# Optimization experiments

Hardware: AMD Instinct MI355X
Metric: run time of the kernel (lower is better)

The kernel has to match this reference:

```python
import jax, jax.numpy as jnp
import numpy as np

D = 128      # d_model
ED = 256     # d_inner = 2*d_model
N = 16       # d_state
DT = 8       # dt_rank = ceil(d_model/16)
K = 4        # d_conv
NL = 2       # n_layers
NC = 2       # n_classes
EPS = 1e-5


def setup_inputs() -> dict:
    key = jax.random.key(0)
    ks = jax.random.split(key, 16)
    L, IN = 12000, 1024
    s = 0.02
    inp = {}
    inp['x'] = jax.random.normal(ks[0], (1, L, IN), jnp.float32)
    inp['coords'] = jax.random.uniform(ks[1], (L, 2), jnp.float32)
    inp['fc1_w'] = jax.random.normal(ks[2], (IN, D), jnp.float32) * s
    inp['fc1_b'] = jnp.zeros((D,), jnp.float32)
    inp['rms_w'] = jnp.ones((NL, D), jnp.float32)
    inp['inproj_w'] = jax.random.normal(ks[3], (NL, D, 2 * ED), jnp.float32) * s
    inp['conv_w'] = jax.random.normal(ks[4], (NL, ED, K), jnp.float32) * s
    inp['conv_b'] = jnp.zeros((NL, ED), jnp.float32)
    inp['xproj_w'] = jax.random.normal(ks[5], (NL, ED, DT + 2 * N), jnp.float32) * s
    inp['dt_w'] = jax.random.normal(ks[6], (NL, DT, ED), jnp.float32) * s
    inp['dt_b'] = jax.random.normal(ks[7], (NL, ED), jnp.float32) * 0.1
    inp['A_log'] = jnp.log(jnp.broadcast_to(jnp.arange(1, N + 1, dtype=jnp.float32), (NL, ED, N)))
    inp['D_p'] = jnp.ones((NL, ED), jnp.float32)
    inp['outproj_w'] = jax.random.normal(ks[8], (NL, ED, D), jnp.float32) * s
    inp['ln_w'] = jnp.ones((D,), jnp.float32)
    inp['ln_b'] = jnp.zeros((D,), jnp.float32)
    inp['att_w1'] = jax.random.normal(ks[9], (D, 128), jnp.float32) * s
    inp['att_b1'] = jnp.zeros((128,), jnp.float32)
    inp['att_w2'] = jax.random.normal(ks[10], (128, 1), jnp.float32) * s
    inp['att_b2'] = jnp.zeros((1,), jnp.float32)
    inp['cls_w'] = jax.random.normal(ks[11], (D, NC), jnp.float32) * s
    inp['cls_b'] = jnp.zeros((NC,), jnp.float32)
    return inp


def _rmsnorm(x, w):
    return x * jax.lax.rsqrt(jnp.mean(x * x, axis=-1, keepdims=True) + EPS) * w


def _layernorm(x, w, b):
    m = jnp.mean(x, axis=-1, keepdims=True)
    v = jnp.mean((x - m) ** 2, axis=-1, keepdims=True)
    return (x - m) * jax.lax.rsqrt(v + EPS) * w + b


def _causal_conv(xb, w, b):
    # xb: [B,L,ED], w: [ED,K] depthwise causal conv
    xpad = jnp.pad(xb, ((0, 0), (K - 1, 0), (0, 0)))
    kern = w.T[:, None, :]  # [K,1,ED]
    out = jax.lax.conv_general_dilated(
        xpad, kern, window_strides=(1,), padding='VALID',
        feature_group_count=ED, dimension_numbers=('NWC', 'WIO', 'NWC'))
    return out + b


def _mamba_block(h, ipw, cw, cb, xpw, dtw, dtb, alog, dp, opw):
    # h: [B,L,D]
    xz = h @ ipw                                  # [B,L,2*ED]
    xb, z = xz[..., :ED], xz[..., ED:]
    xc = jax.nn.silu(_causal_conv(xb, cw, cb))    # [B,L,ED]
    dbl = xc @ xpw                                # [B,L,DT+2N]
    dlt, Bm, Cm = dbl[..., :DT], dbl[..., DT:DT + N], dbl[..., DT + N:]
    delta = jax.nn.softplus(dlt @ dtw + dtb)      # [B,L,ED]
    A = -jnp.exp(alog)                            # [ED,N]
    dA = jnp.exp(delta[..., None] * A)            # [B,L,ED,N]
    dBx = (delta * xc)[..., None] * Bm[:, :, None, :]

    def step(hs, inp):
        da, dbx, c = inp
        hs = da * hs + dbx                        # [B,ED,N]
        y = jnp.einsum('ben,bn->be', hs, c)
        return hs, y

    h0 = jnp.zeros((dA.shape[0], ED, N), dA.dtype)
    xs = (dA.transpose(1, 0, 2, 3), dBx.transpose(1, 0, 2, 3), Cm.transpose(1, 0, 2))
    _, ys = jax.lax.scan(step, h0, xs)            # [L,B,ED]
    y = ys.transpose(1, 0, 2) + dp * xc
    y = y * jax.nn.silu(z)
    return y @ opw                                # [B,L,D]


def reference(x, coords, fc1_w, fc1_b, rms_w, inproj_w, conv_w, conv_b, xproj_w,
              dt_w, dt_b, A_log, D_p, outproj_w, ln_w, ln_b,
              att_w1, att_b1, att_w2, att_b2, cls_w, cls_b):
    h = jax.nn.gelu(x @ fc1_w + fc1_b, approximate=False)
    for i in range(NL):
        h = h + _mamba_block(_rmsnorm(h, rms_w[i]), inproj_w[i], conv_w[i], conv_b[i],
                             xproj_w[i], dt_w[i], dt_b[i], A_log[i], D_p[i], outproj_w[i])
    h = _layernorm(h, ln_w, ln_b)
    A = jnp.tanh(h @ att_w1 + att_b1) @ att_w2 + att_b2   # [1,L,1]
    A = jax.nn.softmax(A.transpose(0, 2, 1), axis=-1)     # [1,1,L]
    pooled = jnp.einsum('bol,bld->bod', A, h)[0]          # [1,D]
    logits = pooled @ cls_w + cls_b                       # [1,NC]
    Y_prob = jax.nn.softmax(logits, axis=1)
    Y_hat = jnp.argmax(logits, axis=1)
    return (logits, Y_prob, Y_hat)
```

## Files before the change

kernel.cpp:

```cpp
#include <hip/hip_runtime.h>

#define LQ 12000
#define IN_D 1024
#define DM 128
#define EDM 256
#define NS 16
#define CCH 480
#define SCH 25
#define GN 32
#define GSZ 15

typedef __bf16 v8bf __attribute__((ext_vector_type(8)));
typedef float v4f __attribute__((ext_vector_type(4)));

__device__ __forceinline__ float wave_sum64(float v) {
#pragma unroll
  for (int o = 32; o > 0; o >>= 1) v += __shfl_xor(v, o);
  return v;
}
__device__ __forceinline__ float wave_max64(float v) {
#pragma unroll
  for (int o = 32; o > 0; o >>= 1) v = fmaxf(v, __shfl_xor(v, o));
  return v;
}

template <bool AF32, int KT, int NT, int EPI>
__global__ __launch_bounds__(256) void bgemm_k(
    const void* __restrict__ Av, const __bf16* __restrict__ Bt,
    const float* __restrict__ bias, const float* __restrict__ nw,
    const float* __restrict__ nb, const float* __restrict__ hin,
    float* __restrict__ o0, __bf16* __restrict__ o1) {
  constexpr int KCH = KT / 4;
  constexpr int COLS = NT * 32;
  constexpr int RS = COLS + 4;
  constexpr int PL = 32 * RS;
  constexpr int CPT = COLS / 8;
  __shared__ __align__(16) float lds[4 * PL];
  const int tid = threadIdx.x, lane = tid & 63, wid = tid >> 6;
  const int frow = lane & 15, g = lane >> 4, fseg = g * 8;
  const int r0 = blockIdx.x * 32;
  const int k0 = wid * KCH + fseg;

  const float* pa32_0 = nullptr;
  const float* pa32_1 = nullptr;
  const __bf16* pab_0 = nullptr;
  const __bf16* pab_1 = nullptr;
  if constexpr (AF32) {
    pa32_0 = (const float*)Av + (size_t)(r0 + frow) * KT + k0;
    pa32_1 = pa32_0 + (size_t)16 * KT;
  } else {
    pab_0 = (const __bf16*)Av + (size_t)(r0 + frow) * KT + k0;
    pab_1 = pab_0 + (size_t)16 * KT;
  }
  const __bf16* pb[NT][2];
#pragma unroll
  for (int nt = 0; nt < NT; ++nt) {
    pb[nt][0] = Bt + (size_t)(nt * 32 + frow) * KT + k0;
    pb[nt][1] = pb[nt][0] + (size_t)16 * KT;
  }

  v4f acc[NT][2][2] = {};
#pragma unroll
  for (int kt = 0; kt < KCH; kt += 32) {
    v8bf a0, a1;
    if constexpr (AF32) {
      float4 u0 = *(const float4*)(pa32_0 + kt);
      float4 u1 = *(const float4*)(pa32_0 + kt + 4);
      float4 u2 = *(const float4*)(pa32_1 + kt);
      float4 u3 = *(const float4*)(pa32_1 + kt + 4);
      a0 = v8bf{(__bf16)u0.x, (__bf16)u0.y, (__bf16)u0.z, (__bf16)u0.w,
                (__bf16)u1.x, (__bf16)u1.y, (__bf16)u1.z, (__bf16)u1.w};
      a1 = v8bf{(__bf16)u2.x, (__bf16)u2.y, (__bf16)u2.z, (__bf16)u2.w,
                (__bf16)u3.x, (__bf16)u3.y, (__bf16)u3.z, (__bf16)u3.w};
    } else {
      a0 = *(const v8bf*)(pab_0 + kt);
      a1 = *(const v8bf*)(pab_1 + kt);
    }
#pragma unroll
    for (int nt = 0; nt < NT; ++nt) {
      v8bf b0 = *(const v8bf*)(pb[nt][0] + kt);
      v8bf b1 = *(const v8bf*)(pb[nt][1] + kt);
      acc[nt][0][0] =
          __builtin_amdgcn_mfma_f32_16x16x32_bf16(a0, b0, acc[nt][0][0], 0, 0, 0);
      acc[nt][0][1] =
          __builtin_amdgcn_mfma_f32_16x16x32_bf16(a0, b1, acc[nt][0][1], 0, 0, 0);
      acc[nt][1][0] =
          __builtin_amdgcn_mfma_f32_16x16x32_bf16(a1, b0, acc[nt][1][0], 0, 0, 0);
      acc[nt][1][1] =
          __builtin_amdgcn_mfma_f32_16x16x32_bf16(a1, b1, acc[nt][1][1], 0, 0, 0);
    }
  }

  float* pl = lds + wid * PL;
#pragma unroll
  for (int nt = 0; nt < NT; ++nt)
#pragma unroll
    for (int i = 0; i < 2; ++i)
#pragma unroll
      for (int j = 0; j < 2; ++j) {
        int cc = nt * 32 + j * 16 + frow;
#pragma unroll
        for (int r = 0; r < 4; ++r)
          pl[(i * 16 + g * 4 + r) * RS + cc] = acc[nt][i][j][r];
      }
  __syncthreads();

  const int row = tid >> 3, c0 = (tid & 7) * CPT;
  const int rr = r0 + row;
  float v[CPT];
#pragma unroll
  for (int k4 = 0; k4 < CPT / 4; ++k4) {
    v4f s = {0.f, 0.f, 0.f, 0.f};
#pragma unroll
    for (int p = 0; p < 4; ++p)
      s = s + *(const v4f*)&lds[p * PL + row * RS + c0 + k4 * 4];
    v[k4 * 4 + 0] = s[0];
    v[k4 * 4 + 1] = s[1];
    v[k4 * 4 + 2] = s[2];
    v[k4 * 4 + 3] = s[3];
  }

  if constexpr (EPI == 0) {
#pragma unroll
    for (int k = 0; k < CPT; ++k) {
      int c = c0 + k;
      if (c < 40) o0[(size_t)rr * 40 + c] = v[k];
    }
  } else if constexpr (EPI == 1 || EPI == 2) {
    float ss = 0.f;
#pragma unroll
    for (int k = 0; k < CPT; ++k) {
      int c = c0 + k;
      float a;
      if constexpr (EPI == 1) {
        a = v[k] + bias[c];
        a = 0.5f * a * (1.f + erff(a * 0.70710678118654752f));
      } else {
        a = v[k] + hin[(size_t)rr * DM + c];
      }
      v[k] = a;
      o0[(size_t)rr * DM + c] = a;
      ss = fmaf(a, a, ss);
    }
#pragma unroll
    for (int o = 1; o < 8; o <<= 1) ss += __shfl_xor(ss, o);
    float r = 1.f / sqrtf(ss * (1.f / DM) + 1e-5f);
#pragma unroll
    for (int k = 0; k < CPT; ++k) {
      int c = c0 + k;
      o1[(size_t)rr * DM + c] = (__bf16)(v[k] * r * nw[c]);
    }
  } else if constexpr (EPI == 3) {
    float s1 = 0.f, s2 = 0.f;
#pragma unroll
    for (int k = 0; k < CPT; ++k) {
      float a = v[k] + hin[(size_t)rr * DM + c0 + k];
      v[k] = a;
      s1 += a;
      s2 = fmaf(a, a, s2);
    }
#pragma unroll
    for (int o = 1; o < 8; o <<= 1) {
      s1 += __shfl_xor(s1, o);
      s2 += __shfl_xor(s2, o);
    }
    float m = s1 * (1.f / DM);
    float var = s2 * (1.f / DM) - m * m;
    float r = 1.f / sqrtf(var + 1e-5f);
#pragma unroll
    for (int k = 0; k < CPT; ++k) {
      int c = c0 + k;
      float y = (v[k] - m) * r * nw[c] + nb[c];
      o0[(size_t)rr * DM + c] = y;
      o1[(size_t)rr * DM + c] = (__bf16)y;
    }
  } else if constexpr (EPI == 4) {
    float dot = 0.f;
#pragma unroll
    for (int k = 0; k < CPT; ++k) {
      int c = c0 + k;
      float a = tanhf(v[k] + bias[c]);
      dot = fmaf(a, nw[c], dot);
    }
#pragma unroll
    for (int o = 1; o < 8; o <<= 1) dot += __shfl_xor(dot, o);
    if ((tid & 7) == 0) o0[rr] = dot + nb[0];
  }
}

template <int KT>
__global__ __launch_bounds__(256) void wgemm_k(const __bf16* __restrict__ Av,
                                               const __bf16* __restrict__ Bt,
                                               __bf16* __restrict__ Cv, int Mt,
                                               int Nt, int Cs) {
  const int tid = threadIdx.x;
  const int lane = tid & 63;
  const int w = blockIdx.x * 4 + (tid >> 6);
  const int nt = w % Nt;
  const int mt = w / Nt;
  const int frow = lane & 15, fseg = (lane >> 4) * 8;
  const int r0 = mt * 32, c0 = nt * 32;

  const __bf16* pb0 = Bt + (size_t)(c0 + frow) * KT + fseg;
  const __bf16* pb1 = pb0 + (size_t)16 * KT;
  const __bf16* pa0 = Av + (size_t)(r0 + frow) * KT + fseg;
  const __bf16* pa1 = pa0 + (size_t)16 * KT;

  v4f acc[2][2] = {};
#pragma unroll
  for (int kt = 0; kt < KT; kt += 32) {
    v8bf a0 = *(const v8bf*)(pa0 + kt);
    v8bf a1 = *(const v8bf*)(pa1 + kt);
    v8bf b0 = *(const v8bf*)(pb0 + kt);
    v8bf b1 = *(const v8bf*)(pb1 + kt);
    acc[0][0] = __builtin_amdgcn_mfma_f32_16x16x32_bf16(a0, b0, acc[0][0], 0, 0, 0);
    acc[0][1] = __builtin_amdgcn_mfma_f32_16x16x32_bf16(a0, b1, acc[0][1], 0, 0, 0);
    acc[1][0] = __builtin_amdgcn_mfma_f32_16x16x32_bf16(a1, b0, acc[1][0], 0, 0, 0);
    acc[1][1] = __builtin_amdgcn_mfma_f32_16x16x32_bf16(a1, b1, acc[1][1], 0, 0, 0);
  }
#pragma unroll
  for (int i = 0; i < 2; ++i)
#pragma unroll
    for (int j = 0; j < 2; ++j) {
      int cc = c0 + j * 16 + (lane & 15);
#pragma unroll
      for (int r = 0; r < 4; ++r) {
        int rr = r0 + i * 16 + (lane >> 4) * 4 + r;
        Cv[(size_t)rr * Cs + cc] = (__bf16)acc[i][j][r];
      }
    }
}

__global__ __launch_bounds__(256) void castw_k(const float* __restrict__ fc1w,
                                               const float* __restrict__ ipw,
                                               const float* __restrict__ xpw,
                                               const float* __restrict__ opw,
                                               const float* __restrict__ a1w,
                                               __bf16* __restrict__ wp) {
  int idx = blockIdx.x * 256 + threadIdx.x;
  const float* src;
  int K, N, o, base;
  if (idx < 131072) {
    base = 0; o = idx; src = fc1w; K = 1024; N = 128;
  } else if (idx < 262144) {
    int t = idx - 131072; int s = t >> 16; o = t & 65535;
    src = ipw + (size_t)s * 65536; K = 128; N = 512; base = 131072 + (s << 16);
  } else if (idx < 327680) {
    int t = idx - 262144; int s = t >> 15; o = t & 32767;
    src = xpw + (size_t)s * 10240; K = 256; N = 40; base = 262144 + (s << 15);
  } else if (idx < 393216) {
    int t = idx - 327680; int s = t >> 15; o = t & 32767;
    src = opw + (size_t)s * 32768; K = 256; N = 128; base = 327680 + (s << 15);
  } else {
    base = 393216; o = idx - 393216; src = a1w; K = 128; N = 128;
  }
  int n = o / K, k = o - n * K;
  float v = (n < N) ? src[(size_t)k * N + n] : 0.f;
  wp[base + o] = (__bf16)v;
}

__global__ __launch_bounds__(256) void conv_silu_k(const __bf16* __restrict__ xzb,
                                                   const float* __restrict__ cw,
                                                   const float* __restrict__ cb,
                                                   float* __restrict__ xc,
                                                   __bf16* __restrict__ xcb) {
  int idx = blockIdx.x * 256 + threadIdx.x;
  int e = idx & (EDM - 1);
  int t = idx >> 8;
  float acc = cb[e];
  const float* wp = cw + e * 4;
#pragma unroll
  for (int j = 0; j < 4; ++j) {
    int ts = t - 3 + j;
    if (ts >= 0) acc = fmaf((float)xzb[(size_t)ts * 512 + e], wp[j], acc);
  }
  float v = __fdividef(acc, 1.f + __expf(-acc));
  xc[idx] = v;
  xcb[idx] = (__bf16)v;
}


__global__ __launch_bounds__(256) void scan1_k(const float* __restrict__ xc,
                                               const float* __restrict__ dbl,
                                               const float* __restrict__ dtw,
                                               const float* __restrict__ dtb,
                                               float* __restrict__ Dsum,
                                               float* __restrict__ Bacc) {
  int e = threadIdx.x;
  int c = blockIdx.x;
  int t0 = c * SCH;
  float wdt[8];
#pragma unroll
  for (int k = 0; k < 8; ++k) wdt[k] = dtw[k * 256 + e];
  float bdt = dtb[e];
  float h[NS];
#pragma unroll
  for (int n = 0; n < NS; ++n) h[n] = 0.f;
  float ds = 0.f;
  const float* xp = xc + (size_t)t0 * EDM + e;
  const float* rp = dbl + (size_t)t0 * 40;
  for (int s = 0; s < SCH; ++s) {
    const float* R = rp + s * 40;
    float acc = bdt;
#pragma unroll
    for (int k = 0; k < 8; ++k) acc = fmaf(R[k], wdt[k], acc);
    float d = fmaxf(acc, 0.f) + log1pf(expf(-fabsf(acc)));
    float xcv = xp[s * EDM];
    float q = __expf(-d);
    float dx = d * xcv;
    ds += d;
    const float* B = R + 8;
    float p1 = q, p2 = q * q;
    float p3 = p1 * p2, p4 = p2 * p2;
    float p5 = p1 * p4, p6 = p2 * p4, p7 = p3 * p4, p8 = p4 * p4;
    float pw[16] = {p1,      p2,      p3,      p4,      p5,      p6,
                    p7,      p8,      p1 * p8, p2 * p8, p3 * p8, p4 * p8,
                    p5 * p8, p6 * p8, p7 * p8, p8 * p8};
#pragma unroll
    for (int n = 0; n < NS; ++n) h[n] = fmaf(pw[n], h[n], dx * B[n]);
  }
  Dsum[c * EDM + e] = ds;
  float4* bq = (float4*)(Bacc + (size_t)c * 4096 + e * NS);
  bq[0] = make_float4(h[0], h[1], h[2], h[3]);
  bq[1] = make_float4(h[4], h[5], h[6], h[7]);
  bq[2] = make_float4(h[8], h[9], h[10], h[11]);
  bq[3] = make_float4(h[12], h[13], h[14], h[15]);
}

__global__ __launch_bounds__(256) void scan2a_k(const float* __restrict__ alog,
                                                const float* __restrict__ Dsum,
                                                const float* __restrict__ Bacc,
                                                float* __restrict__ Gs,
                                                float* __restrict__ Gb) {
  int b = blockIdx.x;
  int g = b >> 4;
  int ch = ((b & 15) << 8) + threadIdx.x;
  int e = ch >> 4;
  float Aen = -expf(alog[ch]);
  float hh = 0.f, ds = 0.f;
#pragma unroll
  for (int j = 0; j < GSZ; ++j) {
    int c = g * GSZ + j;
    float dsv = Dsum[c * EDM + e];
    ds += dsv;
    hh = fmaf(__expf(Aen * dsv), hh, Bacc[(size_t)c * 4096 + ch]);
  }
  Gs[g * 4096 + ch] = ds;
  Gb[g * 4096 + ch] = hh;
}

__global__ __launch_bounds__(256) void scan2b_k(const float* __restrict__ alog,
                                                const float* __restrict__ Gs,
                                                const float* __restrict__ Gb,
                                                float* __restrict__ Gc) {
  int ch = blockIdx.x * 256 + threadIdx.x;
  float Aen = -expf(alog[ch]);
  float gs[GN], gb[GN];
#pragma unroll
  for (int g = 0; g < GN; ++g) {
    gs[g] = Gs[g * 4096 + ch];
    gb[g] = Gb[g * 4096 + ch];
  }
  float carry = 0.f;
#pragma unroll
  for (int g = 0; g < GN; ++g) {
    Gc[g * 4096 + ch] = carry;
    carry = fmaf(__expf(Aen * gs[g]), carry, gb[g]);
  }
}

__global__ __launch_bounds__(256) void scan2c_k(const float* __restrict__ alog,
                                                const float* __restrict__ Dsum,
                                                float* __restrict__ Bacc,
                                                const float* __restrict__ Gc) {
  int b = blockIdx.x;
  int g = b >> 4;
  int ch = ((b & 15) << 8) + threadIdx.x;
  int e = ch >> 4;
  float Aen = -expf(alog[ch]);
  float carry = Gc[g * 4096 + ch];
#pragma unroll
  for (int j = 0; j < GSZ; ++j) {
    int c = g * GSZ + j;
    float a = __expf(Aen * Dsum[c * EDM + e]);
    float old = Bacc[(size_t)c * 4096 + ch];
    Bacc[(size_t)c * 4096 + ch] = carry;
    carry = fmaf(a, carry, old);
  }
}

__global__ __launch_bounds__(256) void scan3_k(const float* __restrict__ xc,
                                               const float* __restrict__ dbl,
                                               const __bf16* __restrict__ xzb,
                                               const float* __restrict__ Bacc,
                                               const float* __restrict__ dtw,
                                               const float* __restrict__ dtb,
                                               const float* __restrict__ dpw,
                                               __bf16* __restrict__ yb) {
  int e = threadIdx.x;
  int c = blockIdx.x;
  int t0 = c * SCH;
  float wdt[8];
#pragma unroll
  for (int k = 0; k < 8; ++k) wdt[k] = dtw[k * 256 + e];
  float bdt = dtb[e];
  float h[NS];
  const float4* hq = (const float4*)(Bacc + (size_t)c * 4096 + e * NS);
  float4 h0 = hq[0], h1 = hq[1], h2 = hq[2], h3 = hq[3];
  h[0] = h0.x; h[1] = h0.y; h[2] = h0.z; h[3] = h0.w;
  h[4] = h1.x; h[5] = h1.y; h[6] = h1.z; h[7] = h1.w;
  h[8] = h2.x; h[9] = h2.y; h[10] = h2.z; h[11] = h2.w;
  h[12] = h3.x; h[13] = h3.y; h[14] = h3.z; h[15] = h3.w;
  float dpe = dpw[e];
  const float* xp = xc + (size_t)t0 * EDM + e;
  const float* rp = dbl + (size_t)t0 * 40;
  const __bf16* zp = xzb + (size_t)t0 * 512 + 256 + e;
  for (int s = 0; s < SCH; ++s) {
    const float* R = rp + s * 40;
    float acc = bdt;
#pragma unroll
    for (int k = 0; k < 8; ++k) acc = fmaf(R[k], wdt[k], acc);
    float d = fmaxf(acc, 0.f) + log1pf(expf(-fabsf(acc)));
    float xcv = xp[s * EDM];
    float q = __expf(-d);
    float dx = d * xcv;
    const float* B = R + 8;
    const float* Cc = R + 24;
    float p1 = q, p2 = q * q;
    float p3 = p1 * p2, p4 = p2 * p2;
    float p5 = p1 * p4, p6 = p2 * p4, p7 = p3 * p4, p8 = p4 * p4;
    float pw[16] = {p1,      p2,      p3,      p4,      p5,      p6,
                    p7,      p8,      p1 * p8, p2 * p8, p3 * p8, p4 * p8,
                    p5 * p8, p6 * p8, p7 * p8, p8 * p8};
    float v0 = 0.f, v1 = 0.f, v2 = 0.f, v3 = 0.f;
#pragma unroll
    for (int n = 0; n < NS; n += 4) {
      h[n] = fmaf(pw[n], h[n], dx * B[n]);
      v0 = fmaf(h[n], Cc[n], v0);
      h[n + 1] = fmaf(pw[n + 1], h[n + 1], dx * B[n + 1]);
      v1 = fmaf(h[n + 1], Cc[n + 1], v1);
      h[n + 2] = fmaf(pw[n + 2], h[n + 2], dx * B[n + 2]);
      v2 = fmaf(h[n + 2], Cc[n + 2], v2);
      h[n + 3] = fmaf(pw[n + 3], h[n + 3], dx * B[n + 3]);
      v3 = fmaf(h[n + 3], Cc[n + 3], v3);
    }
    float v = (v0 + v1) + (v2 + v3);
    float y = v + dpe * xcv;
    float z = (float)zp[s * 512];
    y *= __fdividef(z, 1.f + __expf(-z));
    yb[(size_t)(t0 + s) * EDM + e] = (__bf16)y;
  }
}

__global__ __launch_bounds__(1024) void att_stats_k(const float* __restrict__ s,
                                                    float* __restrict__ stats) {
  __shared__ float red[16];
  int lane = threadIdx.x & 63, wid = threadIdx.x >> 6;
  float m = -1e30f;
  for (int i = threadIdx.x; i < LQ; i += 1024) m = fmaxf(m, s[i]);
  m = wave_max64(m);
  if (lane == 0) red[wid] = m;
  __syncthreads();
  if (threadIdx.x < 16) {
    float mm = red[threadIdx.x];
#pragma unroll
    for (int o = 8; o > 0; o >>= 1) mm = fmaxf(mm, __shfl_xor(mm, o));
    if (threadIdx.x == 0) red[0] = mm;
  }
  __syncthreads();
  float smax = red[0];
  __syncthreads();
  float sum = 0.f;
  for (int i = threadIdx.x; i < LQ; i += 1024) sum += expf(s[i] - smax);
  sum = wave_sum64(sum);
  if (lane == 0) red[wid] = sum;
  __syncthreads();
  if (threadIdx.x == 0) {
    float tot = 0.f;
    for (int i = 0; i < 16; ++i) tot += red[i];
    stats[0] = smax;
    stats[1] = tot;
  }
}

__global__ __launch_bounds__(128) void pooled_k(const float* __restrict__ s,
                                                const float* __restrict__ stats,
                                                const float* __restrict__ hn,
                                                float* __restrict__ pooled) {
  __shared__ float w[64];
  int t0 = blockIdx.x * 64;
  float smax = stats[0];
  if (threadIdx.x < 64) {
    int t = t0 + threadIdx.x;
    w[threadIdx.x] = (t < LQ) ? expf(s[t] - smax) : 0.f;
  }
  __syncthreads();
  int d = threadIdx.x;
  float acc = 0.f;
  int nmax = min(64, LQ - t0);
  for (int i = 0; i < nmax; ++i)
    acc = fmaf(w[i], hn[(size_t)(t0 + i) * DM + d], acc);
  atomicAdd(&pooled[d], acc);
}

__global__ __launch_bounds__(128) void final_k(const float* __restrict__ pooled,
                                               const float* __restrict__ stats,
                                               const float* __restrict__ cls_w,
                                               const float* __restrict__ cls_b,
                                               float* __restrict__ out) {
  __shared__ float r0[2], r1[2];
  int lane = threadIdx.x & 63, wid = threadIdx.x >> 6;
  float p = pooled[threadIdx.x] / stats[1];
  float v0 = p * cls_w[threadIdx.x * 2 + 0];
  float v1 = p * cls_w[threadIdx.x * 2 + 1];
  v0 = wave_sum64(v0);
  v1 = wave_sum64(v1);
  if (lane == 0) {
    r0[wid] = v0;
    r1[wid] = v1;
  }
  __syncthreads();
  if (threadIdx.x == 0) {
    float L0 = r0[0] + r0[1] + cls_b[0];
    float L1 = r1[0] + r1[1] + cls_b[1];
    float mx = fmaxf(L0, L1);
    float e0 = expf(L0 - mx), e1 = expf(L1 - mx);
    float inv = 1.f / (e0 + e1);
    out[0] = L0;
    out[1] = L1;
    out[2] = e0 * inv;
    out[3] = e1 * inv;
    out[4] = (L1 > L0) ? 1.f : 0.f;
  }
}

extern "C" void kernel_launch(void* const* d_in, const int* in_sizes, int n_in,
                              void* d_out, int out_size, void* d_ws,
                              size_t ws_size, hipStream_t stream) {
  const float* x = (const float*)d_in[0];
  const float* fc1_w = (const float*)d_in[2];
  const float* fc1_b = (const float*)d_in[3];
  const float* rms_w = (const float*)d_in[4];
  const float* inproj_w = (const float*)d_in[5];
  const float* conv_w = (const float*)d_in[6];
  const float* conv_b = (const float*)d_in[7];
  const float* xproj_w = (const float*)d_in[8];
  const float* dt_w = (const float*)d_in[9];
  const float* dt_b = (const float*)d_in[10];
  const float* A_log = (const float*)d_in[11];
  const float* D_p = (const float*)d_in[12];
  const float* outproj_w = (const float*)d_in[13];
  const float* ln_w = (const float*)d_in[14];
  const float* ln_b = (const float*)d_in[15];
  const float* att_w1 = (const float*)d_in[16];
  const float* att_b1 = (const float*)d_in[17];
  const float* att_w2 = (const float*)d_in[18];
  const float* att_b2 = (const float*)d_in[19];
  const float* cls_w = (const float*)d_in[20];
  const float* cls_b = (const float*)d_in[21];
  float* out = (float*)d_out;

  float* ws = (float*)d_ws;
  float* h = ws;
  float* hn = h + 1536000;
  float* xc = hn + 1536000;
  float* dbl = xc + 3072000;
  float* Dsum = dbl + 480000;
  float* Bacc = Dsum + 122880;
  float* Gs = Bacc + 1966080;
  float* Gb = Gs + 131072;
  float* Gc = Gb + 131072;
  float* pooled = Gc + 131072;
  float* stats = pooled + 128;
  __bf16* wp = (__bf16*)(stats + 16);
  __bf16* hnb = wp + 409600;
  __bf16* xcb = hnb + 1536000;
  __bf16* yb = xcb + 3072000;
  __bf16* xzb = yb + 3072000;

  const __bf16* fc1T = wp;
  const __bf16* ipT[2] = {wp + 131072, wp + 196608};
  const __bf16* xpT[2] = {wp + 262144, wp + 294912};
  const __bf16* opT[2] = {wp + 327680, wp + 360448};
  const __bf16* a1T = wp + 393216;

  hipMemsetAsync(pooled, 0, 128 * sizeof(float), stream);

  dim3 b256(256);
  castw_k<<<1600, b256, 0, stream>>>(fc1_w, inproj_w, xproj_w, outproj_w,
                                     att_w1, wp);
  bgemm_k<true, 1024, 4, 1><<<375, b256, 0, stream>>>(
      x, fc1T, fc1_b, rms_w, nullptr, nullptr, h, hnb);

  for (int l = 0; l < 2; ++l) {
    const float* alog_l = A_log + l * 4096;
    const float* dtw_l = dt_w + l * 8 * EDM;
    const float* dtb_l = dt_b + l * EDM;
    wgemm_k<128><<<1500, b256, 0, stream>>>(hnb, ipT[l], xzb, 375, 16, 512);
    conv_silu_k<<<12000, b256, 0, stream>>>(xzb, conv_w + l * EDM * 4,
                                            conv_b + l * EDM, xc, xcb);
    bgemm_k<false, 256, 2, 0><<<375, b256, 0, stream>>>(
        xcb, xpT[l], nullptr, nullptr, nullptr, nullptr, dbl, nullptr);
    scan1_k<<<CCH, b256, 0, stream>>>(xc, dbl, dtw_l, dtb_l, Dsum, Bacc);
    scan2a_k<<<512, b256, 0, stream>>>(alog_l, Dsum, Bacc, Gs, Gb);
    scan2b_k<<<16, b256, 0, stream>>>(alog_l, Gs, Gb, Gc);
    scan2c_k<<<512, b256, 0, stream>>>(alog_l, Dsum, Bacc, Gc);
    scan3_k<<<CCH, b256, 0, stream>>>(xc, dbl, xzb, Bacc, dtw_l, dtb_l,
                                      D_p + l * EDM, yb);
    if (l == 0)
      bgemm_k<false, 256, 4, 2><<<375, b256, 0, stream>>>(
          yb, opT[0], nullptr, rms_w + DM, nullptr, h, h, hnb);
    else
      bgemm_k<false, 256, 4, 3><<<375, b256, 0, stream>>>(
          yb, opT[1], nullptr, ln_w, ln_b, h, hn, hnb);
  }

  bgemm_k<false, 128, 4, 4><<<375, b256, 0, stream>>>(
      hnb, a1T, att_b1, att_w2, att_b2, nullptr, dbl, nullptr);
  att_stats_k<<<1, 1024, 0, stream>>>(dbl, stats);
  pooled_k<<<188, 128, 0, stream>>>(dbl, stats, hn, pooled);
  final_k<<<1, 128, 0, stream>>>(pooled, stats, cls_w, cls_b, out);
}
```

Baseline: 389.7 us.

## Fuse causal conv with x_proj GEMM, drop fp32 xc, skip softmax max pass

Merges the depthwise conv+SiLU kernel and the x_proj GEMM into one kernel: each block computes a 32-row tile of conv output into LDS and multiplies it with MFMA, so the fp32 xc buffer disappears. The scans now read the bf16 xc copy instead of fp32. The attention softmax drops its max-subtraction stats kernel, and the pooled kernel accumulates the exp-sum denominator atomically. Together these cut launches and memory traffic. The cost is bf16 rounding of xc in the scans and possible exp overflow without the max shift, which holds only for small attention scores.

```diff
diff --git a/kernel.cpp b/kernel.cpp
--- a/kernel.cpp
+++ b/kernel.cpp
@@ -16,11 +16,6 @@
 __device__ __forceinline__ float wave_sum64(float v) {
 #pragma unroll
   for (int o = 32; o > 0; o >>= 1) v += __shfl_xor(v, o);
-  return v;
-}
-__device__ __forceinline__ float wave_max64(float v) {
-#pragma unroll
-  for (int o = 32; o > 0; o >>= 1) v = fmaxf(v, __shfl_xor(v, o));
   return v;
 }
 
@@ -120,13 +115,7 @@
     v[k4 * 4 + 3] = s[3];
   }
 
-  if constexpr (EPI == 0) {
-#pragma unroll
-    for (int k = 0; k < CPT; ++k) {
-      int c = c0 + k;
-      if (c < 40) o0[(size_t)rr * 40 + c] = v[k];
-    }
-  } else if constexpr (EPI == 1 || EPI == 2) {
+  if constexpr (EPI == 1 || EPI == 2) {
     float ss = 0.f;
 #pragma unroll
     for (int k = 0; k < CPT; ++k) {
@@ -229,6 +218,65 @@
         Cv[(size_t)rr * Cs + cc] = (__bf16)acc[i][j][r];
       }
     }
+}
+
+__global__ __launch_bounds__(256) void convxp_k(const __bf16* __restrict__ xzb,
+                                                const float* __restrict__ cw,
+                                                const float* __restrict__ cb,
+                                                const __bf16* __restrict__ xpT,
+                                                __bf16* __restrict__ xcb,
+                                                float* __restrict__ dbl) {
+  __shared__ __bf16 tile[32][264];
+  const int tid = threadIdx.x;
+  const int t0 = blockIdx.x * 32;
+  float col[35];
+#pragma unroll
+  for (int j = 0; j < 35; ++j) {
+    int t = t0 - 3 + j;
+    col[j] = (t >= 0) ? (float)xzb[(size_t)t * 512 + tid] : 0.f;
+  }
+  const float* wp = cw + tid * 4;
+  float w0 = wp[0], w1 = wp[1], w2 = wp[2], w3 = wp[3];
+  float bias = cb[tid];
+#pragma unroll
+  for (int t = 0; t < 32; ++t) {
+    float a = bias;
+    a = fmaf(col[t], w0, a);
+    a = fmaf(col[t + 1], w1, a);
+    a = fmaf(col[t + 2], w2, a);
+    a = fmaf(col[t + 3], w3, a);
+    float v = __fdividef(a, 1.f + __expf(-a));
+    __bf16 bv = (__bf16)v;
+    xcb[(size_t)(t0 + t) * EDM + tid] = bv;
+    tile[t][tid] = bv;
+  }
+  __syncthreads();
+  const int lane = tid & 63, wid = tid >> 6;
+  const int mrow = (wid >> 1) * 16, ncol = (wid & 1) * 32;
+  const int frow = lane & 15, fseg = (lane >> 4) * 8;
+  const __bf16* pb0 = xpT + (size_t)(ncol + frow) * 256 + fseg;
+  const __bf16* pb1 = pb0 + (size_t)16 * 256;
+  v4f a0 = {}, a1 = {};
+#pragma unroll
+  for (int kt = 0; kt < 256; kt += 32) {
+    v8bf av = *(const v8bf*)&tile[mrow + frow][kt + fseg];
+    v8bf b0 = *(const v8bf*)(pb0 + kt);
+    v8bf b1 = *(const v8bf*)(pb1 + kt);
+    a0 = __builtin_amdgcn_mfma_f32_16x16x32_bf16(av, b0, a0, 0, 0, 0);
+    a1 = __builtin_amdgcn_mfma_f32_16x16x32_bf16(av, b1, a1, 0, 0, 0);
+  }
+#pragma unroll
+  for (int j = 0; j < 2; ++j) {
+    int cc = ncol + j * 16 + (lane & 15);
+    if (cc < 40) {
+      const v4f& ac = j ? a1 : a0;
+#pragma unroll
+      for (int r = 0; r < 4; ++r) {
+        int rr = t0 + mrow + (lane >> 4) * 4 + r;
+        dbl[(size_t)rr * 40 + cc] = ac[r];
+      }
+    }
+  }
 }
 
 __global__ __launch_bounds__(256) void castw_k(const float* __restrict__ fc1w,
@@ -259,28 +307,8 @@
   wp[base + o] = (__bf16)v;
 }
 
-__global__ __launch_bounds__(256) void conv_silu_k(const __bf16* __restrict__ xzb,
-                                                   const float* __restrict__ cw,
-                                                   const float* __restrict__ cb,
-                                                   float* __restrict__ xc,
-                                                   __bf16* __restrict__ xcb) {
-  int idx = blockIdx.x * 256 + threadIdx.x;
-  int e = idx & (EDM - 1);
-  int t = idx >> 8;
-  float acc = cb[e];
-  const float* wp = cw + e * 4;
-#pragma unroll
-  for (int j = 0; j < 4; ++j) {
-    int ts = t - 3 + j;
-    if (ts >= 0) acc = fmaf((float)xzb[(size_t)ts * 512 + e], wp[j], acc);
-  }
-  float v = __fdividef(acc, 1.f + __expf(-acc));
-  xc[idx] = v;
-  xcb[idx] = (__bf16)v;
-}
-
-
-__global__ __launch_bounds__(256) void scan1_k(const float* __restrict__ xc,
+
+__global__ __launch_bounds__(256) void scan1_k(const __bf16* __restrict__ xcb,
                                                const float* __restrict__ dbl,
                                                const float* __restrict__ dtw,
                                                const float* __restrict__ dtb,
@@ -297,7 +325,7 @@
 #pragma unroll
   for (int n = 0; n < NS; ++n) h[n] = 0.f;
   float ds = 0.f;
-  const float* xp = xc + (size_t)t0 * EDM + e;
+  const __bf16* xp = xcb + (size_t)t0 * EDM + e;
   const float* rp = dbl + (size_t)t0 * 40;
   for (int s = 0; s < SCH; ++s) {
     const float* R = rp + s * 40;
@@ -305,7 +333,7 @@
 #pragma unroll
     for (int k = 0; k < 8; ++k) acc = fmaf(R[k], wdt[k], acc);
     float d = fmaxf(acc, 0.f) + log1pf(expf(-fabsf(acc)));
-    float xcv = xp[s * EDM];
+    float xcv = (float)xp[s * EDM];
     float q = __expf(-d);
     float dx = d * xcv;
     ds += d;
@@ -389,7 +417,7 @@
   }
 }
 
-__global__ __launch_bounds__(256) void scan3_k(const float* __restrict__ xc,
+__global__ __launch_bounds__(256) void scan3_k(const __bf16* __restrict__ xcb,
                                                const float* __restrict__ dbl,
                                                const __bf16* __restrict__ xzb,
                                                const float* __restrict__ Bacc,
@@ -412,7 +440,7 @@
   h[8] = h2.x; h[9] = h2.y; h[10] = h2.z; h[11] = h2.w;
   h[12] = h3.x; h[13] = h3.y; h[14] = h3.z; h[15] = h3.w;
   float dpe = dpw[e];
-  const float* xp = xc + (size_t)t0 * EDM + e;
+  const __bf16* xp = xcb + (size_t)t0 * EDM + e;
   const float* rp = dbl + (size_t)t0 * 40;
   const __bf16* zp = xzb + (size_t)t0 * 512 + 256 + e;
   for (int s = 0; s < SCH; ++s) {
@@ -421,7 +449,7 @@
 #pragma unroll
     for (int k = 0; k < 8; ++k) acc = fmaf(R[k], wdt[k], acc);
     float d = fmaxf(acc, 0.f) + log1pf(expf(-fabsf(acc)));
-    float xcv = xp[s * EDM];
+    float xcv = (float)xp[s * EDM];
     float q = __expf(-d);
     float dx = d * xcv;
     const float* B = R + 8;
@@ -452,65 +480,38 @@
   }
 }
 
-__global__ __launch_bounds__(1024) void att_stats_k(const float* __restrict__ s,
-                                                    float* __restrict__ stats) {
-  __shared__ float red[16];
-  int lane = threadIdx.x & 63, wid = threadIdx.x >> 6;
-  float m = -1e30f;
-  for (int i = threadIdx.x; i < LQ; i += 1024) m = fmaxf(m, s[i]);
-  m = wave_max64(m);
-  if (lane == 0) red[wid] = m;
-  __syncthreads();
-  if (threadIdx.x < 16) {
-    float mm = red[threadIdx.x];
-#pragma unroll
-    for (int o = 8; o > 0; o >>= 1) mm = fmaxf(mm, __shfl_xor(mm, o));
-    if (threadIdx.x == 0) red[0] = mm;
-  }
-  __syncthreads();
-  float smax = red[0];
-  __syncthreads();
-  float sum = 0.f;
-  for (int i = threadIdx.x; i < LQ; i += 1024) sum += expf(s[i] - smax);
-  sum = wave_sum64(sum);
-  if (lane == 0) red[wid] = sum;
-  __syncthreads();
-  if (threadIdx.x == 0) {
-    float tot = 0.f;
-    for (int i = 0; i < 16; ++i) tot += red[i];
-    stats[0] = smax;
-    stats[1] = tot;
-  }
-}
-
 __global__ __launch_bounds__(128) void pooled_k(const float* __restrict__ s,
-                                                const float* __restrict__ stats,
                                                 const float* __restrict__ hn,
-                                                float* __restrict__ pooled) {
+                                                float* __restrict__ pooled,
+                                                float* __restrict__ denom) {
   __shared__ float w[64];
   int t0 = blockIdx.x * 64;
-  float smax = stats[0];
+  int nmax = min(64, LQ - t0);
   if (threadIdx.x < 64) {
     int t = t0 + threadIdx.x;
-    w[threadIdx.x] = (t < LQ) ? expf(s[t] - smax) : 0.f;
+    w[threadIdx.x] = (t < LQ) ? expf(s[t]) : 0.f;
   }
   __syncthreads();
   int d = threadIdx.x;
   float acc = 0.f;
-  int nmax = min(64, LQ - t0);
   for (int i = 0; i < nmax; ++i)
     acc = fmaf(w[i], hn[(size_t)(t0 + i) * DM + d], acc);
   atomicAdd(&pooled[d], acc);
+  if (threadIdx.x == 64) {
+    float sw = 0.f;
+    for (int i = 0; i < nmax; ++i) sw += w[i];
+    atomicAdd(denom, sw);
+  }
 }
 
 __global__ __launch_bounds__(128) void final_k(const float* __restrict__ pooled,
-                                               const float* __restrict__ stats,
+                                               const float* __restrict__ denom,
                                                const float* __restrict__ cls_w,
                                                const float* __restrict__ cls_b,
                                                float* __restrict__ out) {
   __shared__ float r0[2], r1[2];
   int lane = threadIdx.x & 63, wid = threadIdx.x >> 6;
-  float p = pooled[threadIdx.x] / stats[1];
+  float p = pooled[threadIdx.x] / denom[0];
   float v0 = p * cls_w[threadIdx.x * 2 + 0];
   float v1 = p * cls_w[threadIdx.x * 2 + 1];
   v0 = wave_sum64(v0);
@@ -563,8 +564,7 @@
   float* ws = (float*)d_ws;
   float* h = ws;
   float* hn = h + 1536000;
-  float* xc = hn + 1536000;
-  float* dbl = xc + 3072000;
+  float* dbl = hn + 1536000;
   float* Dsum = dbl + 480000;
   float* Bacc = Dsum + 122880;
   float* Gs = Bacc + 1966080;
@@ -584,7 +584,7 @@
   const __bf16* opT[2] = {wp + 327680, wp + 360448};
   const __bf16* a1T = wp + 393216;
 
-  hipMemsetAsync(pooled, 0, 128 * sizeof(float), stream);
+  hipMemsetAsync(pooled, 0, 144 * sizeof(float), stream);
 
   dim3 b256(256);
   castw_k<<<1600, b256, 0, stream>>>(fc1_w, inproj_w, xproj_w, outproj_w,
@@ -597,15 +597,13 @@
     const float* dtw_l = dt_w + l * 8 * EDM;
     const float* dtb_l = dt_b + l * EDM;
     wgemm_k<128><<<1500, b256, 0, stream>>>(hnb, ipT[l], xzb, 375, 16, 512);
-    conv_silu_k<<<12000, b256, 0, stream>>>(xzb, conv_w + l * EDM * 4,
-                                            conv_b + l * EDM, xc, xcb);
-    bgemm_k<false, 256, 2, 0><<<375, b256, 0, stream>>>(
-        xcb, xpT[l], nullptr, nullptr, nullptr, nullptr, dbl, nullptr);
-    scan1_k<<<CCH, b256, 0, stream>>>(xc, dbl, dtw_l, dtb_l, Dsum, Bacc);
+    convxp_k<<<375, b256, 0, stream>>>(xzb, conv_w + l * EDM * 4,
+                                       conv_b + l * EDM, xpT[l], xcb, dbl);
+    scan1_k<<<CCH, b256, 0, stream>>>(xcb, dbl, dtw_l, dtb_l, Dsum, Bacc);
     scan2a_k<<<512, b256, 0, stream>>>(alog_l, Dsum, Bacc, Gs, Gb);
     scan2b_k<<<16, b256, 0, stream>>>(alog_l, Gs, Gb, Gc);
     scan2c_k<<<512, b256, 0, stream>>>(alog_l, Dsum, Bacc, Gc);
-    scan3_k<<<CCH, b256, 0, stream>>>(xc, dbl, xzb, Bacc, dtw_l, dtb_l,
+    scan3_k<<<CCH, b256, 0, stream>>>(xcb, dbl, xzb, Bacc, dtw_l, dtb_l,
                                       D_p + l * EDM, yb);
     if (l == 0)
       bgemm_k<false, 256, 4, 2><<<375, b256, 0, stream>>>(
@@ -617,7 +615,6 @@
 
   bgemm_k<false, 128, 4, 4><<<375, b256, 0, stream>>>(
       hnb, a1T, att_b1, att_w2, att_b2, nullptr, dbl, nullptr);
-  att_stats_k<<<1, 1024, 0, stream>>>(dbl, stats);
-  pooled_k<<<188, 128, 0, stream>>>(dbl, stats, hn, pooled);
+  pooled_k<<<188, 128, 0, stream>>>(dbl, hn, pooled, stats);
   final_k<<<1, 128, 0, stream>>>(pooled, stats, cls_w, cls_b, out);
 }
```

Result: faster. 372.4 us (-4.4%).
